# Optimization experiments

Hardware: AMD Instinct MI355X
Metric: run time of the kernel (lower is better)

The kernel has to match this reference:

```python
import jax, jax.numpy as jnp
import numpy as np

B, M, C, IMG, P, D, L, H, DFF, NC = 16, 4, 3, 224, 16, 768, 12, 12, 3072, 1000
G = IMG // P
S = G * G + 1
HD = D // H
EPS = 1e-6
SCALE = HD ** -0.5


def setup_inputs() -> dict:
    key = jax.random.key(0)
    ks = jax.random.split(key, 12)
    w = lambda k, shape: (jax.random.normal(k, shape) * 0.02).astype(jnp.float32)
    return {
        'x': jax.random.normal(ks[0], (B, C, IMG, IMG), jnp.float32),
        'x_tangent': jax.random.normal(ks[1], (B, M, C, IMG, IMG), jnp.float32),
        'patch_w': w(ks[2], (D, C * P * P)), 'patch_b': jnp.zeros((D,), jnp.float32),
        'cls_token': w(ks[3], (1, 1, D)), 'pos_embed': w(ks[4], (1, S, D)),
        'ln1_g': jnp.ones((L, D), jnp.float32), 'ln1_b': jnp.zeros((L, D), jnp.float32),
        'qkv_w': w(ks[5], (L, 3 * D, D)), 'qkv_b': jnp.zeros((L, 3 * D), jnp.float32),
        'proj_w': w(ks[6], (L, D, D)), 'proj_b': jnp.zeros((L, D), jnp.float32),
        'ln2_g': jnp.ones((L, D), jnp.float32), 'ln2_b': jnp.zeros((L, D), jnp.float32),
        'fc1_w': w(ks[7], (L, DFF, D)), 'fc1_b': jnp.zeros((L, DFF), jnp.float32),
        'fc2_w': w(ks[8], (L, D, DFF)), 'fc2_b': jnp.zeros((L, D), jnp.float32),
        'normf_g': jnp.ones((D,), jnp.float32), 'normf_b': jnp.zeros((D,), jnp.float32),
        'head_w': w(ks[9], (NC, D)), 'head_b': jnp.zeros((NC,), jnp.float32),
    }


def _patchify(img):
    # [b,C,IMG,IMG] -> [b, G*G, C*P*P], matching Conv2d(patch) weight layout (c, ph, pw)
    b = img.shape[0]
    p = img.reshape(b, C, G, P, G, P).transpose(0, 2, 4, 1, 3, 5)
    return p.reshape(b, G * G, C * P * P)


def _ln_jvp(x, t, g, b):
    # x: [B,S,D], t: [B,M,S,D]; params constant w.r.t. tangent directions
    mu = x.mean(-1, keepdims=True)
    xc = x - mu
    inv = jax.lax.rsqrt((xc * xc).mean(-1, keepdims=True) + EPS)
    xh = xc * inv
    y = xh * g + b
    xh_b, inv_b = xh[:, None], inv[:, None]
    ty = g * inv_b * (t - t.mean(-1, keepdims=True) - xh_b * (xh_b * t).mean(-1, keepdims=True))
    return y, ty


def _gelu_jvp(x, t):
    # exact (erf) GELU and its derivative; x: [B,S,F], t: [B,M,S,F]
    cdf = 0.5 * (1.0 + jax.lax.erf(x * 0.7071067811865476))
    pdf = jnp.exp(-0.5 * x * x) * 0.3989422804014327
    return x * cdf, t * (cdf + x * pdf)[:, None]


def _softmax_jvp(s, ts):
    # s: [B,H,S,S], ts: [B,M,H,S,S]
    a = jax.nn.softmax(s, axis=-1)
    a_b = a[:, None]
    ta = a_b * (ts - (a_b * ts).sum(-1, keepdims=True))
    return a, ta


def reference(x, x_tangent, patch_w, patch_b, cls_token, pos_embed,
              ln1_g, ln1_b, qkv_w, qkv_b, proj_w, proj_b, ln2_g, ln2_b,
              fc1_w, fc1_b, fc2_w, fc2_b, normf_g, normf_b, head_w, head_b):
    # patch embed (primal + tangent; bias/pos/cls are constants -> zero tangent)
    h = _patchify(x) @ patch_w.T + patch_b                                  # [B,N,D]
    th = (_patchify(x_tangent.reshape(B * M, C, IMG, IMG)) @ patch_w.T).reshape(B, M, G * G, D)
    cls = jnp.broadcast_to(cls_token, (B, 1, D))
    h = jnp.concatenate([cls, h], axis=1) + pos_embed                       # [B,S,D]
    th = jnp.concatenate([jnp.zeros((B, M, 1, D), th.dtype), th], axis=2)   # [B,M,S,D]

    for l in range(L):
        # --- attention (manual JVP, matching the torch einsum path) ---
        y, ty = _ln_jvp(h, th, ln1_g[l], ln1_b[l])
        qkv = y @ qkv_w[l].T + qkv_b[l]
        tqkv = ty @ qkv_w[l].T
        q, k, v = jnp.split(qkv, 3, axis=-1)
        tq, tk, tv = jnp.split(tqkv, 3, axis=-1)
        q = q.reshape(B, S, H, HD); k = k.reshape(B, S, H, HD); v = v.reshape(B, S, H, HD)
        tq = tq.reshape(B, M, S, H, HD); tk = tk.reshape(B, M, S, H, HD); tv = tv.reshape(B, M, S, H, HD)
        s = jnp.einsum('bqhd,bkhd->bhqk', q, k) * SCALE
        ts = (jnp.einsum('bmqhd,bkhd->bmhqk', tq, k)
              + jnp.einsum('bqhd,bmkhd->bmhqk', q, tk)) * SCALE
        a, ta = _softmax_jvp(s, ts)
        o = jnp.einsum('bhqk,bkhd->bqhd', a, v).reshape(B, S, D)
        to = (jnp.einsum('bmhqk,bkhd->bmqhd', ta, v)
              + jnp.einsum('bhqk,bmkhd->bmqhd', a, tv)).reshape(B, M, S, D)
        h = h + o @ proj_w[l].T + proj_b[l]
        th = th + to @ proj_w[l].T
        # --- mlp ---
        y, ty = _ln_jvp(h, th, ln2_g[l], ln2_b[l])
        y = y @ fc1_w[l].T + fc1_b[l]
        ty = ty @ fc1_w[l].T
        y, ty = _gelu_jvp(y, ty)
        h = h + y @ fc2_w[l].T + fc2_b[l]
        th = th + ty @ fc2_w[l].T

    y, ty = _ln_jvp(h, th, normf_g, normf_b)
    logits = y[:, 0] @ head_w.T + head_b            # token pooling
    tlogits = ty[:, :, 0] @ head_w.T                 # [B,M,NC]
    return logits, tlogits
```

## Files before the change

### kernel.cpp

```cpp
#include <hip/hip_runtime.h>
#include <hip/hip_bf16.h>

#define DEVI __device__ __forceinline__

typedef short  bf16x8 __attribute__((ext_vector_type(8)));
typedef float  f32x4  __attribute__((ext_vector_type(4)));

static constexpr int BB   = 16;
static constexpr int MM   = 4;
static constexpr int CC   = 3;
static constexpr int IMG  = 224;
static constexpr int PPP  = 16;
static constexpr int DD   = 768;
static constexpr int LL   = 12;
static constexpr int HH   = 12;
static constexpr int DFF  = 3072;
static constexpr int NCLS = 1000;
static constexpr int GG   = 14;
static constexpr int SS   = 197;
static constexpr int HD   = 64;
static constexpr int BT   = BB*SS;
static constexpr int BMT  = BB*MM*SS;
static constexpr int RT   = BT+BMT;
static constexpr int RP   = 15872;
static constexpr int SP   = 208;
static constexpr int QLD  = 3*DD;
static constexpr int PRP  = BB*GG*GG;
static constexpr int PRT  = (BB+BB*MM)*GG*GG;
static constexpr float EPSV  = 1e-6f;
static constexpr float SCALE = 0.125f;

static constexpr int NQW  = QLD*DD;
static constexpr int NPW  = DD*DD;
static constexpr int NF1W = DFF*DD;
static constexpr int NF2W = DD*DFF;
static constexpr int WTOT = NQW+NPW+NF1W+NF2W;

static constexpr int CH   = 4;
static constexpr int BMC  = (BB*MM)/CH;

DEVI unsigned short f2bf(float x){
  union { float f; unsigned u; } v; v.f = x;
  unsigned r = v.u + 0x7fffu + ((v.u>>16)&1u);
  return (unsigned short)(r>>16);
}
DEVI float bf2f(unsigned short x){
  union { unsigned u; float f; } v; v.u = ((unsigned)x)<<16;
  return v.f;
}
DEVI f32x4 mfma16(bf16x8 a, bf16x8 b, f32x4 c){
  return __builtin_amdgcn_mfma_f32_16x16x32_bf16(a,b,c,0,0,0);
}
typedef const void __attribute__((address_space(1)))* gas1;
typedef void __attribute__((address_space(3)))* las3;


__global__ __launch_bounds__(256) void f2bf_kernel(const float* __restrict__ in,
    unsigned short* __restrict__ out, size_t n){
  size_t i = (size_t)blockIdx.x*256 + threadIdx.x;
  size_t stride = (size_t)gridDim.x*256;
  for (; i<n; i+=stride) out[i] = f2bf(in[i]);
}

__global__ __launch_bounds__(256) void conv_layer(const float* __restrict__ qkvw,
    const float* __restrict__ projw, const float* __restrict__ f1w,
    const float* __restrict__ f2w, unsigned short* __restrict__ wl){
  int i = blockIdx.x*256 + threadIdx.x;
  float v;
  if (i < NQW)                v = qkvw[i];
  else if (i < NQW+NPW)       v = projw[i-NQW];
  else if (i < NQW+NPW+NF1W)  v = f1w[i-NQW-NPW];
  else                        v = f2w[i-NQW-NPW-NF1W];
  wl[i] = f2bf(v);
}

__global__ __launch_bounds__(256) void conv_all(const float* __restrict__ qkvw,
    const float* __restrict__ projw, const float* __restrict__ f1w,
    const float* __restrict__ f2w, unsigned short* __restrict__ wl){
  int l = blockIdx.y;
  int i = blockIdx.x*256 + threadIdx.x;
  float v;
  if (i < NQW)                v = qkvw[(size_t)l*NQW + i];
  else if (i < NQW+NPW)       v = projw[(size_t)l*NPW + (i-NQW)];
  else if (i < NQW+NPW+NF1W)  v = f1w[(size_t)l*NF1W + (i-NQW-NPW)];
  else                        v = f2w[(size_t)l*NF2W + (i-NQW-NPW-NF1W)];
  wl[(size_t)l*WTOT + i] = f2bf(v);
}

__global__ __launch_bounds__(256) void init_h(float* __restrict__ hh,
    const float* __restrict__ cls, const float* __restrict__ pos,
    const float* __restrict__ patch_b){
  size_t i = (size_t)blockIdx.x*256 + threadIdx.x;
  int r = (int)(i/DD), c = (int)(i%DD);
  float v = 0.f;
  if (r < BT){
    int s_ = r % SS;
    v = pos[(size_t)s_*DD + c] + (s_==0 ? cls[c] : patch_b[c]);
  }
  hh[i] = v;
}

__global__ __launch_bounds__(256) void patchify_k(const float* __restrict__ x,
    const float* __restrict__ xt, unsigned short* __restrict__ pat){
  size_t i = (size_t)blockIdx.x*256 + threadIdx.x;
  int r = (int)(i/DD), kk = (int)(i%DD);
  int c = kk>>8, rem = kk&255, py = rem>>4, px = rem&15;
  const float* src;
  if (r < PRP){
    int b_ = r/(GG*GG), p = r%(GG*GG);
    src = x + (((size_t)b_*CC + c)*IMG + (size_t)(p/GG)*PPP + py)*IMG + (p%GG)*PPP + px;
  } else {
    int rr = r-PRP; int bm = rr/(GG*GG), p = rr%(GG*GG);
    src = xt + (((size_t)bm*CC + c)*IMG + (size_t)(p/GG)*PPP + py)*IMG + (p%GG)*PPP + px;
  }
  pat[i] = f2bf(*src);
}


DEVI void blockSum4(float&a,float&b,float&c,float&d,float* red){
  #pragma unroll
  for (int off=32; off; off>>=1){
    a += __shfl_xor(a,off,64); b += __shfl_xor(b,off,64);
    c += __shfl_xor(c,off,64); d += __shfl_xor(d,off,64);
  }
  int w = threadIdx.x>>6;
  if ((threadIdx.x&63)==0){ red[w]=a; red[4+w]=b; red[8+w]=c; red[12+w]=d; }
  __syncthreads();
  a = red[0]+red[1]+red[2]+red[3];
  b = red[4]+red[5]+red[6]+red[7];
  c = red[8]+red[9]+red[10]+red[11];
  d = red[12]+red[13]+red[14]+red[15];
  __syncthreads();
}

__global__ __launch_bounds__(256) void ln_fused(const float* __restrict__ hh,
    const float* __restrict__ g, const float* __restrict__ bb,
    unsigned short* __restrict__ ybf){
  __shared__ float red[16];
  int r = blockIdx.x;
  int t = threadIdx.x;
  unsigned short* y = ybf + (size_t)r*DD;
  if (r < BT){
    const float* x = hh + (size_t)r*DD;
    float x0=x[t], x1=x[t+256], x2=x[t+512];
    float s1=x0+x1+x2, s2=x0*x0+x1*x1+x2*x2, s3=0.f, s4=0.f;
    blockSum4(s1,s2,s3,s4,red);
    float mu  = s1*(1.f/DD);
    float inv = rsqrtf(s2*(1.f/DD) - mu*mu + EPSV);
    y[t]     = f2bf((x0-mu)*inv*g[t]     + bb[t]);
    y[t+256] = f2bf((x1-mu)*inv*g[t+256] + bb[t+256]);
    y[t+512] = f2bf((x2-mu)*inv*g[t+512] + bb[t+512]);
  } else {
    int idx = r-BT;
    int s_ = idx % SS;
    int b_ = (idx / SS) / MM;
    int pr = b_*SS + s_;
    const float* tt = hh + (size_t)r*DD;
    const float* xx = hh + (size_t)pr*DD;
    float t0=tt[t], t1=tt[t+256], t2=tt[t+512];
    float x0=xx[t], x1=xx[t+256], x2=xx[t+512];
    float s1=x0+x1+x2, s2=x0*x0+x1*x1+x2*x2;
    float s3=t0+t1+t2, s4=x0*t0+x1*t1+x2*t2;
    blockSum4(s1,s2,s3,s4,red);
    float mu  = s1*(1.f/DD);
    float inv = rsqrtf(s2*(1.f/DD) - mu*mu + EPSV);
    float tmean = s3*(1.f/DD);
    float dot   = inv*(s4*(1.f/DD) - mu*tmean);
    y[t]     = f2bf(g[t]    *inv*(t0 - tmean - (x0-mu)*inv*dot));
    y[t+256] = f2bf(g[t+256]*inv*(t1 - tmean - (x1-mu)*inv*dot));
    y[t+512] = f2bf(g[t+512]*inv*(t2 - tmean - (x2-mu)*inv*dot));
  }
}

__global__ __launch_bounds__(256) void ln_head(const float* __restrict__ hh,
    const float* __restrict__ g, const float* __restrict__ bb,
    unsigned short* __restrict__ ybf){
  __shared__ float red[16];
  int ri = blockIdx.x;
  int t = threadIdx.x;
  if (ri < BB){
    size_t row = (size_t)ri*SS;
    const float* x = hh + row*DD;
    float x0=x[t], x1=x[t+256], x2=x[t+512];
    float s1=x0+x1+x2, s2=x0*x0+x1*x1+x2*x2, s3=0.f, s4=0.f;
    blockSum4(s1,s2,s3,s4,red);
    float mu  = s1*(1.f/DD);
    float inv = rsqrtf(s2*(1.f/DD) - mu*mu + EPSV);
    unsigned short* y = ybf + row*DD;
    y[t]     = f2bf((x0-mu)*inv*g[t]     + bb[t]);
    y[t+256] = f2bf((x1-mu)*inv*g[t+256] + bb[t+256]);
    y[t+512] = f2bf((x2-mu)*inv*g[t+512] + bb[t+512]);
  } else {
    int t2 = ri - BB;
    size_t row = (size_t)BT + (size_t)t2*SS;
    size_t prow = (size_t)(t2/MM)*SS;
    const float* tt = hh + row*DD;
    const float* xx = hh + prow*DD;
    float t0=tt[t], t1=tt[t+256], t2v=tt[t+512];
    float x0=xx[t], x1=xx[t+256], x2=xx[t+512];
    float s1=x0+x1+x2, s2=x0*x0+x1*x1+x2*x2;
    float s3=t0+t1+t2v, s4=x0*t0+x1*t1+x2*t2v;
    blockSum4(s1,s2,s3,s4,red);
    float mu  = s1*(1.f/DD);
    float inv = rsqrtf(s2*(1.f/DD) - mu*mu + EPSV);
    float tmean = s3*(1.f/DD);
    float dot   = inv*(s4*(1.f/DD) - mu*tmean);
    unsigned short* y = ybf + row*DD;
    y[t]     = f2bf(g[t]    *inv*(t0  - tmean - (x0-mu)*inv*dot));
    y[t+256] = f2bf(g[t+256]*inv*(t1  - tmean - (x1-mu)*inv*dot));
    y[t+512] = f2bf(g[t+512]*inv*(t2v - tmean - (x2-mu)*inv*dot));
  }
}


template<int MODE>
__global__ __launch_bounds__(256,2) void gemm_bt(
    const unsigned short* __restrict__ A,
    const unsigned short* __restrict__ Aalt, int asplit, int lda,
    const unsigned short* __restrict__ W, int K, int N, int Mrows,
    float* __restrict__ outf, unsigned short* __restrict__ outb, int ldc,
    const float* __restrict__ bias, int bias_limit)
{
  __shared__ __attribute__((aligned(16))) unsigned short As[128*64];
  __shared__ __attribute__((aligned(16))) unsigned short Bs[128*64];
  const int tid = threadIdx.x;
  const int wave = tid>>6, lane = tid&63;
  const int nwg  = gridDim.x*gridDim.y;
  const int orig = blockIdx.y*gridDim.x + blockIdx.x;
  const int xcd = orig & 7, i8 = orig >> 3;
  const int qq = nwg >> 3, rr_ = nwg & 7;
  const int wg = (xcd < rr_ ? xcd*(qq+1) : rr_*(qq+1) + (xcd-rr_)*qq) + i8;
  const int tN = wg % gridDim.x, tM = wg / gridDim.x;
  f32x4 acc[4][4];
  f32x4 zf = {0.f,0.f,0.f,0.f};
  #pragma unroll
  for (int m=0;m<4;m++)
    #pragma unroll
    for (int n=0;n<4;n++) acc[m][n] = zf;
  const int wm = wave>>1, wn = wave&1;
  const int lrow = lane&15, lk8 = (lane>>4)<<3;
  const int srow = tid>>3;
  const int scol = (tid&7)<<3;
  const size_t arow0 = (size_t)tM*128;
  const size_t brow0 = (size_t)tN*128;

  for (int k0=0; k0<K; k0+=64){
    #pragma unroll
    for (int i=0;i<4;i++){
      int row = (int)arow0 + srow + i*32;
      const unsigned short* abase = (row < asplit) ? Aalt : A;
      const unsigned short* ga = abase + (size_t)row*lda + (k0+scol);
      __builtin_amdgcn_global_load_lds((gas1)ga, (las3)(As + i*2048 + wave*512), 16, 0, 0);
      const unsigned short* gb = W + (brow0+srow+i*32)*(size_t)K + (k0+scol);
      __builtin_amdgcn_global_load_lds((gas1)gb, (las3)(Bs + i*2048 + wave*512), 16, 0, 0);
    }
    __syncthreads();
    #pragma unroll
    for (int kk=0; kk<64; kk+=32){
      bf16x8 af[4], bw[4];
      #pragma unroll
      for (int m=0;m<4;m++) af[m] = *(const bf16x8*)(As + (wm*64+m*16+lrow)*64 + kk+lk8);
      #pragma unroll
      for (int n=0;n<4;n++) bw[n] = *(const bf16x8*)(Bs + (wn*64+n*16+lrow)*64 + kk+lk8);
      #pragma unroll
      for (int m=0;m<4;m++)
        #pragma unroll
        for (int n=0;n<4;n++)
          acc[m][n] = mfma16(af[m], bw[n], acc[m][n]);
    }
    __syncthreads();
  }

  const int colbase = tN*128 + wn*64 + lrow;
  const int rowbase = tM*128 + wm*64 + ((lane>>4)<<2);
  #pragma unroll
  for (int n=0;n<4;n++){
    int col = colbase + n*16;
    #pragma unroll
    for (int m=0;m<4;m++){
      #pragma unroll
      for (int i=0;i<4;i++){
        int r = rowbase + m*16 + i;
        float v = acc[m][n][i];
        if (MODE==0){
          if (r < bias_limit) v += bias[col];
          outb[(size_t)r*ldc + col] = f2bf(v);
        } else if (MODE==1){
          if (r < Mrows){
            if (r < bias_limit) v += bias[col];
            outf[(size_t)r*ldc + col] += v;
          }
        } else {
          if (r < PRT){
            int orow;
            if (r < PRP) orow = (r/196)*197 + 1 + r%196;
            else { int rr = r-PRP; orow = BT + (rr/196)*197 + 1 + rr%196; }
            outf[(size_t)orow*ldc + col] += v;
          }
        }
      }
    }
  }
}

__global__ __launch_bounds__(256) void transpose_v(const unsigned short* __restrict__ qkv,
    unsigned short* __restrict__ vT, unsigned short* __restrict__ tvT){
  __shared__ unsigned short tile[SP*65];
  int inst = blockIdx.x;
  size_t rowbase; unsigned short* dst; int h;
  if (inst < BB*HH){ int b_=inst/HH; h=inst%HH; rowbase=(size_t)b_*SS; dst = vT + (size_t)inst*HD*SP; }
  else { int i2=inst-BB*HH; int bm=i2/HH; h=i2%HH; rowbase=(size_t)BT+(size_t)bm*SS; dst = tvT + (size_t)i2*HD*SP; }
  int coff = 2*DD + h*HD;
  for (int i=threadIdx.x; i<SP*HD; i+=256){
    int k = i>>6, d = i&63;
    unsigned short v = (k<SS) ? qkv[(rowbase+k)*QLD + coff + d] : (unsigned short)0;
    tile[k*65+d] = v;
  }
  __syncthreads();
  for (int i=threadIdx.x; i<HD*SP; i+=256){
    int d = i/SP, k = i%SP;
    dst[(size_t)d*SP + k] = tile[k*65+d];
  }
}

__global__ __launch_bounds__(256) void attn_s1(const unsigned short* __restrict__ qkv,
                                               unsigned short* __restrict__ abf){
  int qt = blockIdx.x, inst = blockIdx.y;
  int wave = threadIdx.x>>6, lane = threadIdx.x&63;
  int lrow = lane&15, lk = (lane>>4)<<3;
  int q0 = qt*64 + wave*16;
  f32x4 acc[13];
  f32x4 zf = {0.f,0.f,0.f,0.f};
  #pragma unroll
  for (int n=0;n<13;n++) acc[n]=zf;
  int h = inst % HH, b_ = inst / HH;
  size_t prow = (size_t)b_*SS;
  const unsigned short* Ab = qkv + (prow + q0 + lrow)*QLD + h*HD + lk;
  const unsigned short* Bb = qkv + prow*QLD + DD + h*HD + lk;
  #pragma unroll
  for (int kk=0; kk<HD; kk+=32){
    bf16x8 av = *(const bf16x8*)(Ab + kk);
    #pragma unroll
    for (int n=0;n<13;n++){
      bf16x8 bv = *(const bf16x8*)(Bb + (size_t)(n*16+lrow)*QLD + kk);
      acc[n] = mfma16(av, bv, acc[n]);
    }
  }
  int grp = lane>>4;
  unsigned short* obase = abf + (size_t)inst*SP*SP;
  bool okc12 = (lrow < 5);
  #pragma unroll
  for (int i=0;i<4;i++){
    int qr = q0 + grp*4 + i;
    float val[13], e[13];
    float mv = -1e30f;
    #pragma unroll
    for (int n=0;n<13;n++){
      val[n] = acc[n][i]*SCALE;
      if (n<12 || okc12) mv = fmaxf(mv, val[n]);
    }
    #pragma unroll
    for (int off=8; off; off>>=1) mv = fmaxf(mv, __shfl_xor(mv, off, 64));
    float s = 0.f;
    #pragma unroll
    for (int n=0;n<13;n++){
      e[n] = (n<12 || okc12) ? __expf(val[n]-mv) : 0.f;
      s += e[n];
    }
    #pragma unroll
    for (int off=8; off; off>>=1) s += __shfl_xor(s, off, 64);
    float inv = 1.f/s;
    if (qr < SS){
      unsigned short* orow = obase + (size_t)qr*SP;
      #pragma unroll
      for (int n=0;n<13;n++) orow[n*16+lrow] = f2bf(e[n]*inv);
    }
  }
}

__global__ __launch_bounds__(256) void attn_s2(const unsigned short* __restrict__ qkv,
    const unsigned short* __restrict__ abf, unsigned short* __restrict__ tabf,
    int bmix0){
  int qt = blockIdx.x, il = blockIdx.y;
  int wave = threadIdx.x>>6, lane = threadIdx.x&63;
  int lrow = lane&15, lk = (lane>>4)<<3;
  int q0 = qt*64 + wave*16;
  f32x4 acc[13];
  f32x4 zf = {0.f,0.f,0.f,0.f};
  #pragma unroll
  for (int n=0;n<13;n++) acc[n]=zf;
  int h = il % HH;
  int bmix = bmix0 + il / HH;
  int b_ = bmix / MM;
  int bh = b_*HH + h;
  size_t prow = (size_t)b_*SS;
  size_t trow = (size_t)BT + (size_t)bmix*SS;
  #pragma unroll
  for (int p=0;p<2;p++){
    size_t ar = (p==0) ? trow : prow;
    size_t br = (p==1) ? trow : prow;
    const unsigned short* Ab = qkv + (ar + q0 + lrow)*QLD + h*HD + lk;
    const unsigned short* Bb = qkv + br*QLD + DD + h*HD + lk;
    #pragma unroll
    for (int kk=0; kk<HD; kk+=32){
      bf16x8 av = *(const bf16x8*)(Ab + kk);
      #pragma unroll
      for (int n=0;n<13;n++){
        bf16x8 bv = *(const bf16x8*)(Bb + (size_t)(n*16+lrow)*QLD + kk);
        acc[n] = mfma16(av, bv, acc[n]);
      }
    }
  }
  int grp = lane>>4;
  const unsigned short* abase = abf + (size_t)bh*SP*SP;
  unsigned short* tbase = tabf + (size_t)il*SP*SP;
  #pragma unroll
  for (int i=0;i<4;i++){
    int qr = q0 + grp*4 + i;
    int qc = (qr < SS) ? qr : (SS-1);
    const unsigned short* arow = abase + (size_t)qc*SP;
    float av[13], tv[13];
    float dot = 0.f;
    #pragma unroll
    for (int n=0;n<13;n++){
      tv[n] = acc[n][i]*SCALE;
      av[n] = bf2f(arow[n*16+lrow]);
      dot += av[n]*tv[n];
    }
    #pragma unroll
    for (int off=8; off; off>>=1) dot += __shfl_xor(dot, off, 64);
    if (qr < SS){
      unsigned short* trow_ = tbase + (size_t)qr*SP;
      #pragma unroll
      for (int n=0;n<13;n++) trow_[n*16+lrow] = f2bf(av[n]*(tv[n]-dot));
    }
  }
}

template<int NP>
__global__ __launch_bounds__(256) void attn_pv(
    const unsigned short* __restrict__ abf, const unsigned short* __restrict__ tabf,
    const unsigned short* __restrict__ vT,  const unsigned short* __restrict__ tvT,
    unsigned short* __restrict__ obf, int bmix0){
  int qt = blockIdx.x, il = blockIdx.y;
  int wave = threadIdx.x>>6, lane = threadIdx.x&63;
  int lrow = lane&15, lk = (lane>>4)<<3;
  int q0 = qt*64 + wave*16;
  int h = il % HH;
  int bmix = (NP==1) ? (il/HH) : (bmix0 + il/HH);
  int b_ = (NP==1) ? bmix : bmix/MM;
  int bh = b_*HH + h;
  f32x4 acc[4];
  f32x4 zf = {0.f,0.f,0.f,0.f};
  #pragma unroll
  for (int n=0;n<4;n++) acc[n]=zf;
  int arow = q0 + lrow; if (arow > SP-1) arow = SP-1;
  #pragma unroll
  for (int p=0;p<NP;p++){
    const unsigned short* Ab = (NP==2 && p==0) ? tabf + (size_t)il*SP*SP
                                               : abf + (size_t)bh*SP*SP;
    const unsigned short* Bb = (NP==2 && p==1) ? tvT + (size_t)(bmix*HH+h)*HD*SP
                                               : vT + (size_t)bh*HD*SP;
    #pragma unroll
    for (int ks=0; ks<6; ks++){
      int kb = ks*32 + lk;
      bf16x8 av = *(const bf16x8*)(Ab + (size_t)arow*SP + kb);
      #pragma unroll
      for (int n=0;n<4;n++){
        bf16x8 bv = *(const bf16x8*)(Bb + (size_t)(n*16+lrow)*SP + kb);
        acc[n] = mfma16(av, bv, acc[n]);
      }
    }
    {
      int kb = 192 + lk;
      const bf16x8 ZV = {0,0,0,0,0,0,0,0};
      bool ok = (lk < 16);
      bf16x8 av = ok ? *(const bf16x8*)(Ab + (size_t)arow*SP + kb) : ZV;
      #pragma unroll
      for (int n=0;n<4;n++){
        bf16x8 bv = ok ? *(const bf16x8*)(Bb + (size_t)(n*16+lrow)*SP + kb) : ZV;
        acc[n] = mfma16(av, bv, acc[n]);
      }
    }
  }
  size_t orow0 = (NP==1) ? (size_t)bmix*SS : (size_t)BT + (size_t)bmix*SS;
  int qr0 = q0 + ((lane>>4)<<2);
  #pragma unroll
  for (int n=0;n<4;n++){
    int cc = h*HD + n*16 + lrow;
    #pragma unroll
    for (int i=0;i<4;i++){
      int qr = qr0 + i;
      if (qr < SS) obf[(orow0+qr)*DD + cc] = f2bf(acc[n][i]);
    }
  }
}

__global__ __launch_bounds__(256) void gelu_k(unsigned short* __restrict__ fc1o,
                                              unsigned short* __restrict__ pgbf){
  int r = blockIdx.x;
  bool prim = r < BT;
  int pr = 0;
  if (!prim){ int idx = r-BT; int s_ = idx%SS; int b_ = (idx/SS)/MM; pr = b_*SS + s_; }
  bf16x8* base = (bf16x8*)(fc1o + (size_t)r*DFF);
  const bf16x8* pb = (const bf16x8*)(fc1o + (size_t)pr*DFF);
  bf16x8* pg = (bf16x8*)(pgbf + (size_t)r*DFF);
  for (int c = threadIdx.x; c < DFF/8; c += 256){
    if (prim){
      bf16x8 xv = base[c];
      bf16x8 o;
      #pragma unroll
      for (int j=0;j<8;j++){
        float x = bf2f((unsigned short)xv[j]);
        float cdf = 0.5f*(1.f + erff(x*0.70710678118654752f));
        o[j] = (short)f2bf(x*cdf);
      }
      pg[c] = o;
    } else {
      bf16x8 tv8 = base[c];
      bf16x8 xv  = pb[c];
      bf16x8 o;
      #pragma unroll
      for (int j=0;j<8;j++){
        float x  = bf2f((unsigned short)xv[j]);
        float tv = bf2f((unsigned short)tv8[j]);
        float cdf = 0.5f*(1.f + erff(x*0.70710678118654752f));
        float pdf = __expf(-0.5f*x*x)*0.39894228040143267f;
        o[j] = (short)f2bf(tv*(cdf + x*pdf));
      }
      base[c] = o;
    }
  }
}

__global__ __launch_bounds__(256) void head_k(const unsigned short* __restrict__ ybf,
    const float* __restrict__ hw, const float* __restrict__ hb, float* __restrict__ out){
  __shared__ float ysh[DD];
  int ri = blockIdx.x;
  size_t yrow; float* o; bool wb;
  if (ri < BB){ yrow = (size_t)ri*SS; o = out + (size_t)ri*NCLS; wb = true; }
  else { int t2 = ri-BB; yrow = (size_t)BT + (size_t)t2*SS; o = out + (size_t)BB*NCLS + (size_t)t2*NCLS; wb = false; }
  for (int d=threadIdx.x; d<DD; d+=256) ysh[d] = bf2f(ybf[yrow*DD + d]);
  __syncthreads();
  for (int n=threadIdx.x; n<NCLS; n+=256){
    const float* wrow = hw + (size_t)n*DD;
    float acc = wb ? hb[n] : 0.f;
    for (int d=0; d<DD; d++) acc += ysh[d]*wrow[d];
    o[n] = acc;
  }
}

extern "C" void kernel_launch(void* const* d_in, const int* in_sizes, int n_in,
                              void* d_out, int out_size, void* d_ws, size_t ws_size,
                              hipStream_t stream)
{
  const float* x      = (const float*)d_in[0];
  const float* xt     = (const float*)d_in[1];
  const float* patch_w= (const float*)d_in[2];
  const float* patch_b= (const float*)d_in[3];
  const float* cls    = (const float*)d_in[4];
  const float* pos    = (const float*)d_in[5];
  const float* ln1_g  = (const float*)d_in[6];
  const float* ln1_b  = (const float*)d_in[7];
  const float* qkv_w  = (const float*)d_in[8];
  const float* qkv_b  = (const float*)d_in[9];
  const float* proj_w = (const float*)d_in[10];
  const float* proj_b = (const float*)d_in[11];
  const float* ln2_g  = (const float*)d_in[12];
  const float* ln2_b  = (const float*)d_in[13];
  const float* fc1_w  = (const float*)d_in[14];
  const float* fc1_b  = (const float*)d_in[15];
  const float* fc2_w  = (const float*)d_in[16];
  const float* fc2_b  = (const float*)d_in[17];
  const float* nf_g   = (const float*)d_in[18];
  const float* nf_b   = (const float*)d_in[19];
  const float* head_w = (const float*)d_in[20];
  const float* head_b = (const float*)d_in[21];
  float* out = (float*)d_out;

  char* ws = (char*)d_ws;
  size_t off = 0;
  auto alloc = [&](size_t bytes)->char*{
    char* p = ws + off;
    off = (off + bytes + 255) & ~(size_t)255;
    return p;
  };

  unsigned short *w_patch, *wl, *ybf, *qkvbf, *vT, *tvT, *abf, *tabf, *fc1o, *pgbf;
  float *hh;
  auto layout = [&](bool allw)->size_t{
    off = 0;
    w_patch = (unsigned short*)alloc((size_t)DD*DD*2);
    wl      = (unsigned short*)alloc((size_t)WTOT*2*(allw?LL:1));
    hh      = (float*)alloc((size_t)RP*DD*4);
    ybf     = (unsigned short*)alloc((size_t)RP*DD*2);
    size_t slab0 = off;
    qkvbf = (unsigned short*)alloc((size_t)RP*QLD*2);
    vT    = (unsigned short*)alloc((size_t)BB*HH*HD*SP*2);
    tvT   = (unsigned short*)alloc((size_t)BB*MM*HH*HD*SP*2);
    abf   = (unsigned short*)alloc((size_t)BB*HH*SP*SP*2);
    tabf  = (unsigned short*)alloc((size_t)BMC*HH*SP*SP*2);
    size_t endA = off;
    off = slab0;
    fc1o = (unsigned short*)alloc((size_t)RP*DFF*2);
    pgbf = (unsigned short*)alloc((size_t)BT*DFF*2);
    size_t endB = off;
    return (endA > endB) ? endA : endB;
  };
  size_t needAll = layout(true);
  bool allw = (needAll <= ws_size);
  size_t need = allw ? needAll : layout(false);

  if (need > ws_size){
    hipMemsetAsync(d_out, 0x7f, (size_t)out_size*4, stream);
    return;
  }

  dim3 blk(256);
  f2bf_kernel<<<dim3(2304), blk, 0, stream>>>(patch_w, w_patch, (size_t)DD*DD);
  if (allw)
    conv_all<<<dim3(WTOT/256, LL), blk, 0, stream>>>(qkv_w, proj_w, fc1_w, fc2_w, wl);
  init_h<<<dim3((RP*DD)/256), blk, 0, stream>>>(hh, cls, pos, patch_b);
  patchify_k<<<dim3((PRT*DD)/256), blk, 0, stream>>>(x, xt, ybf);
  gemm_bt<2><<<dim3(DD/128, 123), blk, 0, stream>>>(ybf, nullptr, 0, DD, w_patch, DD, DD, PRT,
                                                    hh, nullptr, DD, nullptr, 0);

  for (int l=0; l<LL; l++){
    if (!allw)
      conv_layer<<<dim3(WTOT/256), blk, 0, stream>>>(qkv_w+(size_t)l*NQW, proj_w+(size_t)l*NPW,
                                                     fc1_w+(size_t)l*NF1W, fc2_w+(size_t)l*NF2W, wl);
    const unsigned short* w_qkv = wl + (allw ? (size_t)l*WTOT : 0);
    const unsigned short* w_proj= w_qkv + NQW;
    const unsigned short* w_fc1 = w_qkv + NQW + NPW;
    const unsigned short* w_fc2 = w_qkv + NQW + NPW + NF1W;

    ln_fused<<<dim3(RT), blk, 0, stream>>>(hh, ln1_g+(size_t)l*DD, ln1_b+(size_t)l*DD, ybf);
    gemm_bt<0><<<dim3(QLD/128, RP/128), blk, 0, stream>>>(ybf, nullptr, 0, DD, w_qkv,
        DD, QLD, RT, nullptr, qkvbf, QLD, qkv_b+(size_t)l*QLD, BT);
    transpose_v<<<dim3(BB*HH + BB*MM*HH), blk, 0, stream>>>(qkvbf, vT, tvT);
    attn_s1<<<dim3(4, BB*HH), blk, 0, stream>>>(qkvbf, abf);
    attn_pv<1><<<dim3(4, BB*HH), blk, 0, stream>>>(abf, nullptr, vT, nullptr, ybf, 0);
    for (int c=0; c<CH; c++){
      attn_s2<<<dim3(4, BMC*HH), blk, 0, stream>>>(qkvbf, abf, tabf, c*BMC);
      attn_pv<2><<<dim3(4, BMC*HH), blk, 0, stream>>>(abf, tabf, vT, tvT, ybf, c*BMC);
    }
    gemm_bt<1><<<dim3(DD/128, RP/128), blk, 0, stream>>>(ybf, nullptr, 0, DD, w_proj,
        DD, DD, RT, hh, nullptr, DD, proj_b+(size_t)l*DD, BT);
    ln_fused<<<dim3(RT), blk, 0, stream>>>(hh, ln2_g+(size_t)l*DD, ln2_b+(size_t)l*DD, ybf);
    gemm_bt<0><<<dim3(DFF/128, RP/128), blk, 0, stream>>>(ybf, nullptr, 0, DD, w_fc1,
        DD, DFF, RT, nullptr, fc1o, DFF, fc1_b+(size_t)l*DFF, BT);
    gelu_k<<<dim3(RT), blk, 0, stream>>>(fc1o, pgbf);
    gemm_bt<1><<<dim3(DD/128, RP/128), blk, 0, stream>>>(fc1o, pgbf, BT, DFF, w_fc2,
        DFF, DD, RT, hh, nullptr, DD, fc2_b+(size_t)l*DD, BT);
  }

  ln_head<<<dim3(BB + BB*MM), blk, 0, stream>>>(hh, nf_g, nf_b, ybf);
  head_k<<<dim3(BB + BB*MM), blk, 0, stream>>>(ybf, head_w, head_b, out);
}
```

Before: 8.995 ms.

## Group primal and tangent rows in LN/GELU, vectorize weight conversion, unchunk attention

LayerNorm and GELU kernels now process one primal row together with its four tangent rows per block, so the primal activations are read once instead of five times and the derivative of GELU is computed once. Weight fp32-to-bf16 conversion kernels are vectorized to 8 elements per thread. The tangent attention buffer is sized for all batch-tangent pairs when workspace allows, which removes the 4-way chunking of attn_s2/attn_pv launches. The XCD-aware tile remapping in the GEMM is removed in favor of direct blockIdx mapping, which may hurt L2 locality on the multi-XCD chip.

```diff
diff --git a/kernel.cpp b/kernel.cpp
--- a/kernel.cpp
+++ b/kernel.cpp
@@ -5,6 +5,7 @@
 
 typedef short  bf16x8 __attribute__((ext_vector_type(8)));
 typedef float  f32x4  __attribute__((ext_vector_type(4)));
+typedef float  f32x4v __attribute__((ext_vector_type(4)));
 
 static constexpr int BB   = 16;
 static constexpr int MM   = 4;
@@ -36,9 +37,6 @@
 static constexpr int NF2W = DD*DFF;
 static constexpr int WTOT = NQW+NPW+NF1W+NF2W;
 
-static constexpr int CH   = 4;
-static constexpr int BMC  = (BB*MM)/CH;
-
 DEVI unsigned short f2bf(float x){
   union { float f; unsigned u; } v; v.f = x;
   unsigned r = v.u + 0x7fffu + ((v.u>>16)&1u);
@@ -55,36 +53,44 @@
 typedef void __attribute__((address_space(3)))* las3;
 
 
-__global__ __launch_bounds__(256) void f2bf_kernel(const float* __restrict__ in,
-    unsigned short* __restrict__ out, size_t n){
+DEVI bf16x8 cvt8(const float* src){
+  float4 a = *(const float4*)src;
+  float4 b = *(const float4*)(src+4);
+  bf16x8 o;
+  o[0]=(short)f2bf(a.x); o[1]=(short)f2bf(a.y); o[2]=(short)f2bf(a.z); o[3]=(short)f2bf(a.w);
+  o[4]=(short)f2bf(b.x); o[5]=(short)f2bf(b.y); o[6]=(short)f2bf(b.z); o[7]=(short)f2bf(b.w);
+  return o;
+}
+
+__global__ __launch_bounds__(256) void f2bf8_kernel(const float* __restrict__ in,
+    unsigned short* __restrict__ out, size_t n8){
   size_t i = (size_t)blockIdx.x*256 + threadIdx.x;
-  size_t stride = (size_t)gridDim.x*256;
-  for (; i<n; i+=stride) out[i] = f2bf(in[i]);
-}
-
-__global__ __launch_bounds__(256) void conv_layer(const float* __restrict__ qkvw,
-    const float* __restrict__ projw, const float* __restrict__ f1w,
-    const float* __restrict__ f2w, unsigned short* __restrict__ wl){
-  int i = blockIdx.x*256 + threadIdx.x;
-  float v;
-  if (i < NQW)                v = qkvw[i];
-  else if (i < NQW+NPW)       v = projw[i-NQW];
-  else if (i < NQW+NPW+NF1W)  v = f1w[i-NQW-NPW];
-  else                        v = f2w[i-NQW-NPW-NF1W];
-  wl[i] = f2bf(v);
-}
-
-__global__ __launch_bounds__(256) void conv_all(const float* __restrict__ qkvw,
+  if (i < n8) *(bf16x8*)(out + i*8) = cvt8(in + i*8);
+}
+
+__global__ __launch_bounds__(256) void conv_all_v(const float* __restrict__ qkvw,
     const float* __restrict__ projw, const float* __restrict__ f1w,
     const float* __restrict__ f2w, unsigned short* __restrict__ wl){
   int l = blockIdx.y;
-  int i = blockIdx.x*256 + threadIdx.x;
-  float v;
-  if (i < NQW)                v = qkvw[(size_t)l*NQW + i];
-  else if (i < NQW+NPW)       v = projw[(size_t)l*NPW + (i-NQW)];
-  else if (i < NQW+NPW+NF1W)  v = f1w[(size_t)l*NF1W + (i-NQW-NPW)];
-  else                        v = f2w[(size_t)l*NF2W + (i-NQW-NPW-NF1W)];
-  wl[(size_t)l*WTOT + i] = f2bf(v);
+  size_t i = ((size_t)blockIdx.x*256 + threadIdx.x)*8;
+  const float* src;
+  if (i < NQW)                src = qkvw + (size_t)l*NQW + i;
+  else if (i < NQW+NPW)       src = projw + (size_t)l*NPW + (i-NQW);
+  else if (i < NQW+NPW+NF1W)  src = f1w + (size_t)l*NF1W + (i-NQW-NPW);
+  else                        src = f2w + (size_t)l*NF2W + (i-NQW-NPW-NF1W);
+  *(bf16x8*)(wl + (size_t)l*WTOT + i) = cvt8(src);
+}
+
+__global__ __launch_bounds__(256) void conv_layer_v(const float* __restrict__ qkvw,
+    const float* __restrict__ projw, const float* __restrict__ f1w,
+    const float* __restrict__ f2w, unsigned short* __restrict__ wl){
+  size_t i = ((size_t)blockIdx.x*256 + threadIdx.x)*8;
+  const float* src;
+  if (i < NQW)                src = qkvw + i;
+  else if (i < NQW+NPW)       src = projw + (i-NQW);
+  else if (i < NQW+NPW+NF1W)  src = f1w + (i-NQW-NPW);
+  else                        src = f2w + (i-NQW-NPW-NF1W);
+  *(bf16x8*)(wl + i) = cvt8(src);
 }
 
 __global__ __launch_bounds__(256) void init_h(float* __restrict__ hh,
@@ -133,42 +139,63 @@
   __syncthreads();
 }
 
-__global__ __launch_bounds__(256) void ln_fused(const float* __restrict__ hh,
+__global__ __launch_bounds__(256) void ln_group(const float* __restrict__ hh,
     const float* __restrict__ g, const float* __restrict__ bb,
     unsigned short* __restrict__ ybf){
-  __shared__ float red[16];
+  __shared__ float red[4][10];
   int r = blockIdx.x;
+  int b_ = r/SS, s_ = r%SS;
   int t = threadIdx.x;
-  unsigned short* y = ybf + (size_t)r*DD;
-  if (r < BT){
-    const float* x = hh + (size_t)r*DD;
-    float x0=x[t], x1=x[t+256], x2=x[t+512];
-    float s1=x0+x1+x2, s2=x0*x0+x1*x1+x2*x2, s3=0.f, s4=0.f;
-    blockSum4(s1,s2,s3,s4,red);
-    float mu  = s1*(1.f/DD);
-    float inv = rsqrtf(s2*(1.f/DD) - mu*mu + EPSV);
-    y[t]     = f2bf((x0-mu)*inv*g[t]     + bb[t]);
-    y[t+256] = f2bf((x1-mu)*inv*g[t+256] + bb[t+256]);
-    y[t+512] = f2bf((x2-mu)*inv*g[t+512] + bb[t+512]);
-  } else {
-    int idx = r-BT;
-    int s_ = idx % SS;
-    int b_ = (idx / SS) / MM;
-    int pr = b_*SS + s_;
-    const float* tt = hh + (size_t)r*DD;
-    const float* xx = hh + (size_t)pr*DD;
-    float t0=tt[t], t1=tt[t+256], t2=tt[t+512];
-    float x0=xx[t], x1=xx[t+256], x2=xx[t+512];
-    float s1=x0+x1+x2, s2=x0*x0+x1*x1+x2*x2;
-    float s3=t0+t1+t2, s4=x0*t0+x1*t1+x2*t2;
-    blockSum4(s1,s2,s3,s4,red);
-    float mu  = s1*(1.f/DD);
-    float inv = rsqrtf(s2*(1.f/DD) - mu*mu + EPSV);
-    float tmean = s3*(1.f/DD);
-    float dot   = inv*(s4*(1.f/DD) - mu*tmean);
-    y[t]     = f2bf(g[t]    *inv*(t0 - tmean - (x0-mu)*inv*dot));
-    y[t+256] = f2bf(g[t+256]*inv*(t1 - tmean - (x1-mu)*inv*dot));
-    y[t+512] = f2bf(g[t+512]*inv*(t2 - tmean - (x2-mu)*inv*dot));
+  const float* xx = hh + (size_t)r*DD;
+  float x0=xx[t], x1=xx[t+256], x2=xx[t+512];
+  size_t trow[4];
+  float tv[4][3];
+  #pragma unroll
+  for (int m=0;m<4;m++){
+    trow[m] = (size_t)BT + ((size_t)(b_*MM+m))*SS + s_;
+    const float* tt = hh + trow[m]*DD;
+    tv[m][0]=tt[t]; tv[m][1]=tt[t+256]; tv[m][2]=tt[t+512];
+  }
+  float s[10];
+  s[0]=x0+x1+x2; s[1]=x0*x0+x1*x1+x2*x2;
+  #pragma unroll
+  for (int m=0;m<4;m++){
+    s[2+2*m]=tv[m][0]+tv[m][1]+tv[m][2];
+    s[3+2*m]=x0*tv[m][0]+x1*tv[m][1]+x2*tv[m][2];
+  }
+  #pragma unroll
+  for (int k=0;k<10;k++){
+    float v = s[k];
+    #pragma unroll
+    for (int off=32; off; off>>=1) v += __shfl_xor(v, off, 64);
+    s[k] = v;
+  }
+  int w = t>>6;
+  if ((t&63)==0){
+    #pragma unroll
+    for (int k=0;k<10;k++) red[w][k]=s[k];
+  }
+  __syncthreads();
+  #pragma unroll
+  for (int k=0;k<10;k++) s[k] = red[0][k]+red[1][k]+red[2][k]+red[3][k];
+  float mu  = s[0]*(1.f/DD);
+  float inv = rsqrtf(s[1]*(1.f/DD) - mu*mu + EPSV);
+  float g0=g[t], g1=g[t+256], g2=g[t+512];
+  float h0=(x0-mu)*inv, h1=(x1-mu)*inv, h2=(x2-mu)*inv;
+  {
+    unsigned short* y = ybf + (size_t)r*DD;
+    y[t]     = f2bf(h0*g0 + bb[t]);
+    y[t+256] = f2bf(h1*g1 + bb[t+256]);
+    y[t+512] = f2bf(h2*g2 + bb[t+512]);
+  }
+  #pragma unroll
+  for (int m=0;m<4;m++){
+    float tmean = s[2+2*m]*(1.f/DD);
+    float dot   = inv*(s[3+2*m]*(1.f/DD) - mu*tmean);
+    unsigned short* y = ybf + trow[m]*DD;
+    y[t]     = f2bf(g0*inv*(tv[m][0] - tmean - h0*dot));
+    y[t+256] = f2bf(g1*inv*(tv[m][1] - tmean - h1*dot));
+    y[t+512] = f2bf(g2*inv*(tv[m][2] - tmean - h2*dot));
   }
 }
 
@@ -225,12 +252,7 @@
   __shared__ __attribute__((aligned(16))) unsigned short Bs[128*64];
   const int tid = threadIdx.x;
   const int wave = tid>>6, lane = tid&63;
-  const int nwg  = gridDim.x*gridDim.y;
-  const int orig = blockIdx.y*gridDim.x + blockIdx.x;
-  const int xcd = orig & 7, i8 = orig >> 3;
-  const int qq = nwg >> 3, rr_ = nwg & 7;
-  const int wg = (xcd < rr_ ? xcd*(qq+1) : rr_*(qq+1) + (xcd-rr_)*qq) + i8;
-  const int tN = wg % gridDim.x, tM = wg / gridDim.x;
+  const int tM = blockIdx.y, tN = blockIdx.x;
   f32x4 acc[4][4];
   f32x4 zf = {0.f,0.f,0.f,0.f};
   #pragma unroll
@@ -496,39 +518,36 @@
   }
 }
 
-__global__ __launch_bounds__(256) void gelu_k(unsigned short* __restrict__ fc1o,
-                                              unsigned short* __restrict__ pgbf){
+__global__ __launch_bounds__(256) void gelu_group(unsigned short* __restrict__ fc1o,
+                                                  unsigned short* __restrict__ pgbf){
   int r = blockIdx.x;
-  bool prim = r < BT;
-  int pr = 0;
-  if (!prim){ int idx = r-BT; int s_ = idx%SS; int b_ = (idx/SS)/MM; pr = b_*SS + s_; }
-  bf16x8* base = (bf16x8*)(fc1o + (size_t)r*DFF);
-  const bf16x8* pb = (const bf16x8*)(fc1o + (size_t)pr*DFF);
+  int b_ = r/SS, s_ = r%SS;
+  const bf16x8* pb = (const bf16x8*)(fc1o + (size_t)r*DFF);
   bf16x8* pg = (bf16x8*)(pgbf + (size_t)r*DFF);
+  bf16x8* tb[4];
+  #pragma unroll
+  for (int m=0;m<4;m++)
+    tb[m] = (bf16x8*)(fc1o + ((size_t)BT + (size_t)(b_*MM+m)*SS + s_)*DFF);
   for (int c = threadIdx.x; c < DFF/8; c += 256){
-    if (prim){
-      bf16x8 xv = base[c];
-      bf16x8 o;
-      #pragma unroll
-      for (int j=0;j<8;j++){
-        float x = bf2f((unsigned short)xv[j]);
-        float cdf = 0.5f*(1.f + erff(x*0.70710678118654752f));
-        o[j] = (short)f2bf(x*cdf);
-      }
-      pg[c] = o;
-    } else {
-      bf16x8 tv8 = base[c];
-      bf16x8 xv  = pb[c];
-      bf16x8 o;
-      #pragma unroll
-      for (int j=0;j<8;j++){
-        float x  = bf2f((unsigned short)xv[j]);
-        float tv = bf2f((unsigned short)tv8[j]);
-        float cdf = 0.5f*(1.f + erff(x*0.70710678118654752f));
-        float pdf = __expf(-0.5f*x*x)*0.39894228040143267f;
-        o[j] = (short)f2bf(tv*(cdf + x*pdf));
-      }
-      base[c] = o;
+    bf16x8 xv = pb[c];
+    float deriv[8];
+    bf16x8 o;
+    #pragma unroll
+    for (int j=0;j<8;j++){
+      float x = bf2f((unsigned short)xv[j]);
+      float cdf = 0.5f*(1.f + erff(x*0.70710678118654752f));
+      float pdf = __expf(-0.5f*x*x)*0.39894228040143267f;
+      o[j] = (short)f2bf(x*cdf);
+      deriv[j] = cdf + x*pdf;
+    }
+    pg[c] = o;
+    #pragma unroll
+    for (int m=0;m<4;m++){
+      bf16x8 tv8 = tb[m][c];
+      bf16x8 w;
+      #pragma unroll
+      for (int j=0;j<8;j++) w[j] = (short)f2bf(bf2f((unsigned short)tv8[j])*deriv[j]);
+      tb[m][c] = w;
     }
   }
 }
@@ -588,7 +607,7 @@
 
   unsigned short *w_patch, *wl, *ybf, *qkvbf, *vT, *tvT, *abf, *tabf, *fc1o, *pgbf;
   float *hh;
-  auto layout = [&](bool allw)->size_t{
+  auto layout = [&](bool allw, int nbm)->size_t{
     off = 0;
     w_patch = (unsigned short*)alloc((size_t)DD*DD*2);
     wl      = (unsigned short*)alloc((size_t)WTOT*2*(allw?LL:1));
@@ -599,7 +618,7 @@
     vT    = (unsigned short*)alloc((size_t)BB*HH*HD*SP*2);
     tvT   = (unsigned short*)alloc((size_t)BB*MM*HH*HD*SP*2);
     abf   = (unsigned short*)alloc((size_t)BB*HH*SP*SP*2);
-    tabf  = (unsigned short*)alloc((size_t)BMC*HH*SP*SP*2);
+    tabf  = (unsigned short*)alloc((size_t)nbm*HH*SP*SP*2);
     size_t endA = off;
     off = slab0;
     fc1o = (unsigned short*)alloc((size_t)RP*DFF*2);
@@ -607,19 +626,22 @@
     size_t endB = off;
     return (endA > endB) ? endA : endB;
   };
-  size_t needAll = layout(true);
-  bool allw = (needAll <= ws_size);
-  size_t need = allw ? needAll : layout(false);
-
+
+  bool allw = true; int nbm = BB*MM;
+  size_t need = layout(true, BB*MM);
+  if (need > ws_size){ need = layout(true, BB*MM/4);  allw=true;  nbm=BB*MM/4; }
+  if (need > ws_size){ need = layout(false, BB*MM);   allw=false; nbm=BB*MM;   }
+  if (need > ws_size){ need = layout(false, BB*MM/4); allw=false; nbm=BB*MM/4; }
   if (need > ws_size){
     hipMemsetAsync(d_out, 0x7f, (size_t)out_size*4, stream);
     return;
   }
+  int nch = (BB*MM)/nbm;
 
   dim3 blk(256);
-  f2bf_kernel<<<dim3(2304), blk, 0, stream>>>(patch_w, w_patch, (size_t)DD*DD);
+  f2bf8_kernel<<<dim3((DD*DD/8+255)/256), blk, 0, stream>>>(patch_w, w_patch, (size_t)DD*DD/8);
   if (allw)
-    conv_all<<<dim3(WTOT/256, LL), blk, 0, stream>>>(qkv_w, proj_w, fc1_w, fc2_w, wl);
+    conv_all_v<<<dim3(WTOT/8/256, LL), blk, 0, stream>>>(qkv_w, proj_w, fc1_w, fc2_w, wl);
   init_h<<<dim3((RP*DD)/256), blk, 0, stream>>>(hh, cls, pos, patch_b);
   patchify_k<<<dim3((PRT*DD)/256), blk, 0, stream>>>(x, xt, ybf);
   gemm_bt<2><<<dim3(DD/128, 123), blk, 0, stream>>>(ybf, nullptr, 0, DD, w_patch, DD, DD, PRT,
@@ -627,29 +649,29 @@
 
   for (int l=0; l<LL; l++){
     if (!allw)
-      conv_layer<<<dim3(WTOT/256), blk, 0, stream>>>(qkv_w+(size_t)l*NQW, proj_w+(size_t)l*NPW,
-                                                     fc1_w+(size_t)l*NF1W, fc2_w+(size_t)l*NF2W, wl);
+      conv_layer_v<<<dim3(WTOT/8/256), blk, 0, stream>>>(qkv_w+(size_t)l*NQW, proj_w+(size_t)l*NPW,
+                                                         fc1_w+(size_t)l*NF1W, fc2_w+(size_t)l*NF2W, wl);
     const unsigned short* w_qkv = wl + (allw ? (size_t)l*WTOT : 0);
     const unsigned short* w_proj= w_qkv + NQW;
     const unsigned short* w_fc1 = w_qkv + NQW + NPW;
     const unsigned short* w_fc2 = w_qkv + NQW + NPW + NF1W;
 
-    ln_fused<<<dim3(RT), blk, 0, stream>>>(hh, ln1_g+(size_t)l*DD, ln1_b+(size_t)l*DD, ybf);
+    ln_group<<<dim3(BT), blk, 0, stream>>>(hh, ln1_g+(size_t)l*DD, ln1_b+(size_t)l*DD, ybf);
     gemm_bt<0><<<dim3(QLD/128, RP/128), blk, 0, stream>>>(ybf, nullptr, 0, DD, w_qkv,
         DD, QLD, RT, nullptr, qkvbf, QLD, qkv_b+(size_t)l*QLD, BT);
     transpose_v<<<dim3(BB*HH + BB*MM*HH), blk, 0, stream>>>(qkvbf, vT, tvT);
     attn_s1<<<dim3(4, BB*HH), blk, 0, stream>>>(qkvbf, abf);
     attn_pv<1><<<dim3(4, BB*HH), blk, 0, stream>>>(abf, nullptr, vT, nullptr, ybf, 0);
-    for (int c=0; c<CH; c++){
-      attn_s2<<<dim3(4, BMC*HH), blk, 0, stream>>>(qkvbf, abf, tabf, c*BMC);
-      attn_pv<2><<<dim3(4, BMC*HH), blk, 0, stream>>>(abf, tabf, vT, tvT, ybf, c*BMC);
+    for (int c=0; c<nch; c++){
+      attn_s2<<<dim3(4, nbm*HH), blk, 0, stream>>>(qkvbf, abf, tabf, c*nbm);
+      attn_pv<2><<<dim3(4, nbm*HH), blk, 0, stream>>>(abf, tabf, vT, tvT, ybf, c*nbm);
     }
     gemm_bt<1><<<dim3(DD/128, RP/128), blk, 0, stream>>>(ybf, nullptr, 0, DD, w_proj,
         DD, DD, RT, hh, nullptr, DD, proj_b+(size_t)l*DD, BT);
-    ln_fused<<<dim3(RT), blk, 0, stream>>>(hh, ln2_g+(size_t)l*DD, ln2_b+(size_t)l*DD, ybf);
+    ln_group<<<dim3(BT), blk, 0, stream>>>(hh, ln2_g+(size_t)l*DD, ln2_b+(size_t)l*DD, ybf);
     gemm_bt<0><<<dim3(DFF/128, RP/128), blk, 0, stream>>>(ybf, nullptr, 0, DD, w_fc1,
         DD, DFF, RT, nullptr, fc1o, DFF, fc1_b+(size_t)l*DFF, BT);
-    gelu_k<<<dim3(RT), blk, 0, stream>>>(fc1o, pgbf);
+    gelu_group<<<dim3(BT), blk, 0, stream>>>(fc1o, pgbf);
     gemm_bt<1><<<dim3(DD/128, RP/128), blk, 0, stream>>>(fc1o, pgbf, BT, DFF, w_fc2,
         DFF, DD, RT, hh, nullptr, DD, fc2_b+(size_t)l*DD, BT);
   }
```

Result: faster. 7.969 ms (-11.4%).
